# Kernel optimization log

Hardware: AMD Instinct MI355X
Metric: run time of the kernel (lower is better)

Reference implementation:

```python
import jax, jax.numpy as jnp
import numpy as np

# Dims (match init_kwargs / input_specs)
W_STEPS, E, B, I, F = 128, 16, 64, 8, 64
P = 8 + F  # proj_size = 72


def setup_inputs() -> dict:
    key = jax.random.key(0)
    ks = jax.random.split(key, 8)
    N = B * I
    inputs = jax.random.normal(ks[0], (W_STEPS, E, B, I, F), dtype=jnp.float32)
    state = jnp.zeros((1, E, N, 1), dtype=jnp.float32)
    # linear projection params (xavier-uniform-ish scale)
    lim_lin = np.sqrt(6.0 / (P + F))
    weight_linear = jax.random.uniform(ks[1], (E, P, F), jnp.float32, -lim_lin, lim_lin)
    bias_linear = jnp.zeros((E, P), dtype=jnp.float32)
    # per-ensemble GRU params, hidden_size=1: gate order (r, z, n) as in torch
    lim = 1.0  # torch GRU init: U(-1/sqrt(hidden)=1, 1)
    w_ih = jax.random.uniform(ks[2], (E, 3, P), jnp.float32, -lim, lim)
    w_hh = jax.random.uniform(ks[3], (E, 3), jnp.float32, -lim, lim)
    b_ih = jax.random.uniform(ks[4], (E, 3), jnp.float32, -lim, lim)
    b_hh = jax.random.uniform(ks[5], (E, 3), jnp.float32, -lim, lim)
    return {"inputs": inputs, "state": state, "weight_linear": weight_linear,
            "bias_linear": bias_linear, "w_ih": w_ih, "w_hh": w_hh,
            "b_ih": b_ih, "b_hh": b_hh}


def reference(inputs, state, weight_linear, bias_linear, w_ih, w_hh, b_ih, b_hh):
    W, E_, B_, I_, F_ = inputs.shape
    N = B_ * I_
    x = inputs.reshape(W, E_, N, F_)
    h0 = state[-1].reshape(E_, N)  # hidden_size = 1 -> squeeze last dim
    # y[w,e,n,p] = sum_f weight_linear[e,p,f] * x[w,e,n,f] + bias
    y = jnp.einsum('epf,wenf->wenp', weight_linear, x) + bias_linear[:, None, :]
    # precompute input-side gate activations for all timesteps: (W, E, N, 3)
    gx = jnp.einsum('egp,wenp->weng', w_ih, y) + b_ih[:, None, :]

    def step(h, gxt):
        # hidden-side gates: h (E,N) * w_hh (E,3) -> (E,N,3)
        gh = h[:, :, None] * w_hh[:, None, :] + b_hh[:, None, :]
        r = jax.nn.sigmoid(gxt[..., 0] + gh[..., 0])
        z = jax.nn.sigmoid(gxt[..., 1] + gh[..., 1])
        n = jnp.tanh(gxt[..., 2] + r * gh[..., 2])
        h_new = (1.0 - z) * n + z * h
        return h_new, h_new

    _, outs = jax.lax.scan(step, h0, gx)  # outs: (W, E, N)
    return outs.reshape(W, E_, B_, I_, 1)
```

## Files before the change

### kernel.cpp

```cpp
#include <hip/hip_runtime.h>

#define WD 128
#define ED 16
#define ND 512
#define FD 64
#define PD 72

#define LOG2E  1.44269504088896340736f
#define LOG2E2 2.88539008177792681472f
__device__ __forceinline__ float fast_sig(float x) {
    return __builtin_amdgcn_rcpf(1.0f + __builtin_amdgcn_exp2f(-LOG2E * x));
}
__device__ __forceinline__ float fast_tanh(float x) {
    return 1.0f - 2.0f * __builtin_amdgcn_rcpf(1.0f + __builtin_amdgcn_exp2f(LOG2E2 * x));
}

__global__ __launch_bounds__(64) void gru_prep(
    const float* __restrict__ wl,
    const float* __restrict__ bl,
    const float* __restrict__ wih,
    const float* __restrict__ bih,
    float* __restrict__ ws)
{
    const int eg = blockIdx.x;
    const int e  = eg / 3;
    const int f  = threadIdx.x;

    const float* a = wih + eg * PD;
    const float* w = wl + (size_t)e * PD * FD + f;
    float s = 0.0f;
    #pragma unroll 8
    for (int p = 0; p < PD; ++p) s = fmaf(a[p], w[p * FD], s);
    ws[eg * FD + f] = s;

    const float* b = bl + (size_t)e * PD;
    float pv = a[f] * b[f];
    if (f < 8) pv = fmaf(a[64 + f], b[64 + f], pv);
    pv += __shfl_xor(pv, 1, 64);
    pv += __shfl_xor(pv, 2, 64);
    pv += __shfl_xor(pv, 4, 64);
    pv += __shfl_xor(pv, 8, 64);
    pv += __shfl_xor(pv, 16, 64);
    pv += __shfl_xor(pv, 32, 64);
    if (f == 0) ws[ED * 3 * FD + eg] = pv + bih[eg];
}

__global__ __launch_bounds__(256) void gru_main(
    const float* __restrict__ x,
    const float* __restrict__ st,
    const float* __restrict__ whh,
    const float* __restrict__ bhh,
    const float* __restrict__ ws,
    float* __restrict__ out)
{
    const int lane = threadIdx.x & 63;
    const int gw   = (blockIdx.x << 2) + (threadIdx.x >> 6);
    const int e    = gw >> 7;
    const int r    = lane >> 4;
    const int n    = ((gw & 127) << 2) + r;
    const int c    = lane & 15;

    const float* Wc = ws;
    const float* bc = ws + ED * 3 * FD;

    const float4 w0 = *(const float4*)(Wc + (e * 3 + 0) * FD + c * 4);
    const float4 w1 = *(const float4*)(Wc + (e * 3 + 1) * FD + c * 4);
    const float4 w2 = *(const float4*)(Wc + (e * 3 + 2) * FD + c * 4);
    const float wh0 = whh[e * 3 + 0], wh1 = whh[e * 3 + 1], wh2 = whh[e * 3 + 2];
    const float B0 = bc[e * 3 + 0] + bhh[e * 3 + 0];
    const float B1 = bc[e * 3 + 1] + bhh[e * 3 + 1];
    const float bc2 = bc[e * 3 + 2];
    const float bh2 = bhh[e * 3 + 2];

    float h = st[e * ND + n];

    const float* px = x + ((size_t)e * ND + n) * FD + c * 4;
    const size_t xstr = (size_t)ED * ND * FD;
    float* po = out + (size_t)e * ND + n;
    const size_t ostr = (size_t)ED * ND;

    float4 q0, q1, q2, q3, q4, q5, q6, q7;
    q0 = *(const float4*)px; px += xstr;
    q1 = *(const float4*)px; px += xstr;
    q2 = *(const float4*)px; px += xstr;
    q3 = *(const float4*)px; px += xstr;
    q4 = *(const float4*)px; px += xstr;
    q5 = *(const float4*)px; px += xstr;
    q6 = *(const float4*)px; px += xstr;
    q7 = *(const float4*)px; px += xstr;

#define GRU_STEP(XV)                                                            \
    {                                                                           \
        float s0 = XV.x * w0.x, s1 = XV.x * w1.x, s2 = XV.x * w2.x;             \
        s0 = fmaf(XV.y, w0.y, s0); s1 = fmaf(XV.y, w1.y, s1); s2 = fmaf(XV.y, w2.y, s2); \
        s0 = fmaf(XV.z, w0.z, s0); s1 = fmaf(XV.z, w1.z, s1); s2 = fmaf(XV.z, w2.z, s2); \
        s0 = fmaf(XV.w, w0.w, s0); s1 = fmaf(XV.w, w1.w, s1); s2 = fmaf(XV.w, w2.w, s2); \
        s0 += __shfl_xor(s0, 1, 64); s1 += __shfl_xor(s1, 1, 64); s2 += __shfl_xor(s2, 1, 64); \
        s0 += __shfl_xor(s0, 2, 64); s1 += __shfl_xor(s1, 2, 64); s2 += __shfl_xor(s2, 2, 64); \
        s0 += __shfl_xor(s0, 4, 64); s1 += __shfl_xor(s1, 4, 64); s2 += __shfl_xor(s2, 4, 64); \
        s0 += __shfl_xor(s0, 8, 64); s1 += __shfl_xor(s1, 8, 64); s2 += __shfl_xor(s2, 8, 64); \
        const float rr = fast_sig(s0 + fmaf(h, wh0, B0));                       \
        const float zz = fast_sig(s1 + fmaf(h, wh1, B1));                       \
        const float nn = fast_tanh(fmaf(rr, fmaf(h, wh2, bh2), s2 + bc2));      \
        h = fmaf(zz, h - nn, nn);                                               \
        if (c == 0) *po = h;                                                    \
        po += ostr;                                                             \
    }

    for (int it = 0; it < WD / 8; ++it) {
        const bool pf = it < (WD / 8 - 1);
        { const float4 X = q0; if (pf) { q0 = *(const float4*)px; px += xstr; } GRU_STEP(X); }
        { const float4 X = q1; if (pf) { q1 = *(const float4*)px; px += xstr; } GRU_STEP(X); }
        { const float4 X = q2; if (pf) { q2 = *(const float4*)px; px += xstr; } GRU_STEP(X); }
        { const float4 X = q3; if (pf) { q3 = *(const float4*)px; px += xstr; } GRU_STEP(X); }
        { const float4 X = q4; if (pf) { q4 = *(const float4*)px; px += xstr; } GRU_STEP(X); }
        { const float4 X = q5; if (pf) { q5 = *(const float4*)px; px += xstr; } GRU_STEP(X); }
        { const float4 X = q6; if (pf) { q6 = *(const float4*)px; px += xstr; } GRU_STEP(X); }
        { const float4 X = q7; if (pf) { q7 = *(const float4*)px; px += xstr; } GRU_STEP(X); }
    }
#undef GRU_STEP
}

extern "C" void kernel_launch(void* const* d_in, const int* in_sizes, int n_in,
                              void* d_out, int out_size, void* d_ws, size_t ws_size,
                              hipStream_t stream)
{
    const float* x    = (const float*)d_in[0];
    const float* st   = (const float*)d_in[1];
    const float* wl   = (const float*)d_in[2];
    const float* bl   = (const float*)d_in[3];
    const float* wih  = (const float*)d_in[4];
    const float* whh  = (const float*)d_in[5];
    const float* bih  = (const float*)d_in[6];
    const float* bhh  = (const float*)d_in[7];
    float* out = (float*)d_out;
    float* ws  = (float*)d_ws;

    hipLaunchKernelGGL(gru_prep, dim3(48), dim3(64), 0, stream,
                       wl, bl, wih, bih, ws);
    hipLaunchKernelGGL(gru_main, dim3(512), dim3(256), 0, stream,
                       x, st, whh, bhh, ws, out);
}
```

Measured before the change: 375.4 us.

## Split fused GRU into parallel projection kernel and lightweight scan kernel

Splits the fused kernel in two. The first kernel computes the input-side gate projections for all timesteps with a large grid (2048 blocks) and stores them to a workspace buffer in a scan-friendly layout. The second kernel runs the sequential recurrence with one lane per hidden unit, reading three precomputed gate values per step. This decouples the bandwidth-bound projection from the latency-bound serial chain. The cost is an extra ~12.6 MB write and read of the gate buffer, and the scan kernel launches only 128 single-wave blocks.

```diff
diff --git a/kernel.cpp b/kernel.cpp
--- a/kernel.cpp
+++ b/kernel.cpp
@@ -14,6 +14,8 @@
 __device__ __forceinline__ float fast_tanh(float x) {
     return 1.0f - 2.0f * __builtin_amdgcn_rcpf(1.0f + __builtin_amdgcn_exp2f(LOG2E2 * x));
 }
+
+#define GX_OFF 4096
 
 __global__ __launch_bounds__(64) void gru_prep(
     const float* __restrict__ wl,
@@ -45,80 +47,102 @@
     if (f == 0) ws[ED * 3 * FD + eg] = pv + bih[eg];
 }
 
-__global__ __launch_bounds__(256) void gru_main(
+__global__ __launch_bounds__(256) void gru_proj(
     const float* __restrict__ x,
+    const float* __restrict__ ws,
+    float* __restrict__ gx)
+{
+    const int lane = threadIdx.x & 63;
+    const int wid  = (blockIdx.x << 2) + (threadIdx.x >> 6);
+    const int c    = lane & 15;
+    const int r    = lane >> 4;
+
+    const int R = (wid << 2) + r;
+    const int n = R & (ND - 1);
+    const int e = (R >> 9) & (ED - 1);
+    const int w0i = R >> 13;
+
+    const float* Wc = ws;
+    const float4 wv0 = *(const float4*)(Wc + (e * 3 + 0) * FD + c * 4);
+    const float4 wv1 = *(const float4*)(Wc + (e * 3 + 1) * FD + c * 4);
+    const float4 wv2 = *(const float4*)(Wc + (e * 3 + 2) * FD + c * 4);
+
+    const float* px = x + (size_t)R * FD + c * 4;
+    float* pg = gx + ((size_t)(e * WD + w0i) * 3 + c) * ND + n;
+    const size_t xadv = (size_t)32768 * FD;
+    const size_t gadv = (size_t)4 * 3 * ND;
+
+    float4 X = *(const float4*)px; px += xadv;
+    for (int it = 0; it < 32; ++it) {
+        const float4 Xc = X;
+        if (it < 31) { X = *(const float4*)px; px += xadv; }
+        float s0 = Xc.x * wv0.x, s1 = Xc.x * wv1.x, s2 = Xc.x * wv2.x;
+        s0 = fmaf(Xc.y, wv0.y, s0); s1 = fmaf(Xc.y, wv1.y, s1); s2 = fmaf(Xc.y, wv2.y, s2);
+        s0 = fmaf(Xc.z, wv0.z, s0); s1 = fmaf(Xc.z, wv1.z, s1); s2 = fmaf(Xc.z, wv2.z, s2);
+        s0 = fmaf(Xc.w, wv0.w, s0); s1 = fmaf(Xc.w, wv1.w, s1); s2 = fmaf(Xc.w, wv2.w, s2);
+        s0 += __shfl_xor(s0, 1, 64); s1 += __shfl_xor(s1, 1, 64); s2 += __shfl_xor(s2, 1, 64);
+        s0 += __shfl_xor(s0, 2, 64); s1 += __shfl_xor(s1, 2, 64); s2 += __shfl_xor(s2, 2, 64);
+        s0 += __shfl_xor(s0, 4, 64); s1 += __shfl_xor(s1, 4, 64); s2 += __shfl_xor(s2, 4, 64);
+        s0 += __shfl_xor(s0, 8, 64); s1 += __shfl_xor(s1, 8, 64); s2 += __shfl_xor(s2, 8, 64);
+        float sv = s0;
+        sv = (c == 1) ? s1 : sv;
+        sv = (c == 2) ? s2 : sv;
+        if (c < 3) *pg = sv;
+        pg += gadv;
+    }
+}
+
+__global__ __launch_bounds__(64) void gru_scan(
+    const float* __restrict__ gx,
     const float* __restrict__ st,
     const float* __restrict__ whh,
     const float* __restrict__ bhh,
     const float* __restrict__ ws,
     float* __restrict__ out)
 {
-    const int lane = threadIdx.x & 63;
-    const int gw   = (blockIdx.x << 2) + (threadIdx.x >> 6);
-    const int e    = gw >> 7;
-    const int r    = lane >> 4;
-    const int n    = ((gw & 127) << 2) + r;
-    const int c    = lane & 15;
+    const int lane = threadIdx.x;
+    const int bid  = blockIdx.x;
+    const int e    = bid >> 3;
+    const int n    = ((bid & 7) << 6) + lane;
 
-    const float* Wc = ws;
     const float* bc = ws + ED * 3 * FD;
-
-    const float4 w0 = *(const float4*)(Wc + (e * 3 + 0) * FD + c * 4);
-    const float4 w1 = *(const float4*)(Wc + (e * 3 + 1) * FD + c * 4);
-    const float4 w2 = *(const float4*)(Wc + (e * 3 + 2) * FD + c * 4);
     const float wh0 = whh[e * 3 + 0], wh1 = whh[e * 3 + 1], wh2 = whh[e * 3 + 2];
-    const float B0 = bc[e * 3 + 0] + bhh[e * 3 + 0];
-    const float B1 = bc[e * 3 + 1] + bhh[e * 3 + 1];
+    const float B0  = bc[e * 3 + 0] + bhh[e * 3 + 0];
+    const float B1  = bc[e * 3 + 1] + bhh[e * 3 + 1];
     const float bc2 = bc[e * 3 + 2];
     const float bh2 = bhh[e * 3 + 2];
 
     float h = st[e * ND + n];
+    const float* pg = gx + (size_t)e * WD * 3 * ND + n;
+    float* po = out + (size_t)e * ND + n;
 
-    const float* px = x + ((size_t)e * ND + n) * FD + c * 4;
-    const size_t xstr = (size_t)ED * ND * FD;
-    float* po = out + (size_t)e * ND + n;
-    const size_t ostr = (size_t)ED * ND;
+#define LOADQ(A, B, C, wq) { const float* p_ = pg + (size_t)(wq) * (3 * ND); \
+                             A = p_[0]; B = p_[ND]; C = p_[2 * ND]; }
+#define GSTEP(G0, G1, G2) { \
+        const float rr = fast_sig((G0) + fmaf(h, wh0, B0));                   \
+        const float zz = fast_sig((G1) + fmaf(h, wh1, B1));                   \
+        const float nn = fast_tanh(fmaf(rr, fmaf(h, wh2, bh2), (G2) + bc2));  \
+        h = fmaf(zz, h - nn, nn);                                             \
+        *po = h; po += (size_t)ED * ND; }
 
-    float4 q0, q1, q2, q3, q4, q5, q6, q7;
-    q0 = *(const float4*)px; px += xstr;
-    q1 = *(const float4*)px; px += xstr;
-    q2 = *(const float4*)px; px += xstr;
-    q3 = *(const float4*)px; px += xstr;
-    q4 = *(const float4*)px; px += xstr;
-    q5 = *(const float4*)px; px += xstr;
-    q6 = *(const float4*)px; px += xstr;
-    q7 = *(const float4*)px; px += xstr;
+    float a0,a1,a2, b0,b1,b2, c0,c1,c2, d0,d1,d2,
+          e0,e1,e2, f0,f1,f2, g0,g1,g2, h0,h1,h2;
+    LOADQ(a0,a1,a2, 0); LOADQ(b0,b1,b2, 1); LOADQ(c0,c1,c2, 2); LOADQ(d0,d1,d2, 3);
+    LOADQ(e0,e1,e2, 4); LOADQ(f0,f1,f2, 5); LOADQ(g0,g1,g2, 6); LOADQ(h0,h1,h2, 7);
 
-#define GRU_STEP(XV)                                                            \
-    {                                                                           \
-        float s0 = XV.x * w0.x, s1 = XV.x * w1.x, s2 = XV.x * w2.x;             \
-        s0 = fmaf(XV.y, w0.y, s0); s1 = fmaf(XV.y, w1.y, s1); s2 = fmaf(XV.y, w2.y, s2); \
-        s0 = fmaf(XV.z, w0.z, s0); s1 = fmaf(XV.z, w1.z, s1); s2 = fmaf(XV.z, w2.z, s2); \
-        s0 = fmaf(XV.w, w0.w, s0); s1 = fmaf(XV.w, w1.w, s1); s2 = fmaf(XV.w, w2.w, s2); \
-        s0 += __shfl_xor(s0, 1, 64); s1 += __shfl_xor(s1, 1, 64); s2 += __shfl_xor(s2, 1, 64); \
-        s0 += __shfl_xor(s0, 2, 64); s1 += __shfl_xor(s1, 2, 64); s2 += __shfl_xor(s2, 2, 64); \
-        s0 += __shfl_xor(s0, 4, 64); s1 += __shfl_xor(s1, 4, 64); s2 += __shfl_xor(s2, 4, 64); \
-        s0 += __shfl_xor(s0, 8, 64); s1 += __shfl_xor(s1, 8, 64); s2 += __shfl_xor(s2, 8, 64); \
-        const float rr = fast_sig(s0 + fmaf(h, wh0, B0));                       \
-        const float zz = fast_sig(s1 + fmaf(h, wh1, B1));                       \
-        const float nn = fast_tanh(fmaf(rr, fmaf(h, wh2, bh2), s2 + bc2));      \
-        h = fmaf(zz, h - nn, nn);                                               \
-        if (c == 0) *po = h;                                                    \
-        po += ostr;                                                             \
+    for (int w8 = 0; w8 < WD; w8 += 8) {
+        const bool pf = (w8 + 8) < WD;
+        { const float t0=a0,t1=a1,t2=a2; if (pf) LOADQ(a0,a1,a2, w8+8);  GSTEP(t0,t1,t2); }
+        { const float t0=b0,t1=b1,t2=b2; if (pf) LOADQ(b0,b1,b2, w8+9);  GSTEP(t0,t1,t2); }
+        { const float t0=c0,t1=c1,t2=c2; if (pf) LOADQ(c0,c1,c2, w8+10); GSTEP(t0,t1,t2); }
+        { const float t0=d0,t1=d1,t2=d2; if (pf) LOADQ(d0,d1,d2, w8+11); GSTEP(t0,t1,t2); }
+        { const float t0=e0,t1=e1,t2=e2; if (pf) LOADQ(e0,e1,e2, w8+12); GSTEP(t0,t1,t2); }
+        { const float t0=f0,t1=f1,t2=f2; if (pf) LOADQ(f0,f1,f2, w8+13); GSTEP(t0,t1,t2); }
+        { const float t0=g0,t1=g1,t2=g2; if (pf) LOADQ(g0,g1,g2, w8+14); GSTEP(t0,t1,t2); }
+        { const float t0=h0,t1=h1,t2=h2; if (pf) LOADQ(h0,h1,h2, w8+15); GSTEP(t0,t1,t2); }
     }
-
-    for (int it = 0; it < WD / 8; ++it) {
-        const bool pf = it < (WD / 8 - 1);
-        { const float4 X = q0; if (pf) { q0 = *(const float4*)px; px += xstr; } GRU_STEP(X); }
-        { const float4 X = q1; if (pf) { q1 = *(const float4*)px; px += xstr; } GRU_STEP(X); }
-        { const float4 X = q2; if (pf) { q2 = *(const float4*)px; px += xstr; } GRU_STEP(X); }
-        { const float4 X = q3; if (pf) { q3 = *(const float4*)px; px += xstr; } GRU_STEP(X); }
-        { const float4 X = q4; if (pf) { q4 = *(const float4*)px; px += xstr; } GRU_STEP(X); }
-        { const float4 X = q5; if (pf) { q5 = *(const float4*)px; px += xstr; } GRU_STEP(X); }
-        { const float4 X = q6; if (pf) { q6 = *(const float4*)px; px += xstr; } GRU_STEP(X); }
-        { const float4 X = q7; if (pf) { q7 = *(const float4*)px; px += xstr; } GRU_STEP(X); }
-    }
-#undef GRU_STEP
+#undef LOADQ
+#undef GSTEP
 }
 
 extern "C" void kernel_launch(void* const* d_in, const int* in_sizes, int n_in,
@@ -135,9 +159,12 @@
     const float* bhh  = (const float*)d_in[7];
     float* out = (float*)d_out;
     float* ws  = (float*)d_ws;
+    float* gx  = ws + GX_OFF;
 
     hipLaunchKernelGGL(gru_prep, dim3(48), dim3(64), 0, stream,
                        wl, bl, wih, bih, ws);
-    hipLaunchKernelGGL(gru_main, dim3(512), dim3(256), 0, stream,
-                       x, st, whh, bhh, ws, out);
+    hipLaunchKernelGGL(gru_proj, dim3(2048), dim3(256), 0, stream,
+                       x, ws, gx);
+    hipLaunchKernelGGL(gru_scan, dim3(128), dim3(64), 0, stream,
+                       gx, st, whh, bhh, ws, out);
 }
```

New measurement: 396.0 us. 5.5% more time.
